# Kernel tuning notes

Measured on AMD Instinct MI355X. Metric: run time of the kernel, lower is better.

## Reference

```python
import jax, jax.numpy as jnp
import numpy as np

WS = 7      # window_size
NH = 8      # num_heads
ND = 5      # n_degree -> Np = 6


def setup_inputs() -> dict:
    key = jax.random.key(0)
    ks = jax.random.split(key, 9)
    B, Q, C, H, W = 2, 100, 256, 64, 64
    Np = ND + 1
    ws2 = WS * WS
    return {
        "x": jax.random.normal(ks[0], (B, C, H, W), dtype=jnp.float32),
        "polys": jax.random.uniform(ks[1], (B, Q, 2, Np), dtype=jnp.float32),
        "w_qkv": jax.random.normal(ks[2], (3 * C, C), dtype=jnp.float32) * 0.02,
        "b_qkv": jnp.zeros((3 * C,), dtype=jnp.float32),
        "w_proj": jax.random.normal(ks[3], (C, C), dtype=jnp.float32) * 0.02,
        "b_proj": jnp.zeros((C,), dtype=jnp.float32),
        "conv_w": jax.random.normal(ks[4], (1, ws2, 1, 1), dtype=jnp.float32) * 0.1,
        "conv_b": jnp.zeros((1,), dtype=jnp.float32),
        "pos_bias": jax.random.normal(ks[5], (ws2, 1), dtype=jnp.float32),
    }


def reference(x, polys, w_qkv, b_qkv, w_proj, b_proj, conv_w, conv_b, pos_bias):
    B, C, H, W = x.shape
    _, Q, _, Np = polys.shape  # polys: [B,Q,2,n_degree+1]
    ws = WS
    ws2 = ws * ws
    nh = NH
    hd = C // nh
    scale = hd ** -0.5

    # --- polynomial -> sample points (get_points) ---
    alpha = jnp.linspace(0.0, 1.0, Np)
    alphas = jnp.stack([alpha ** i for i in range(Np - 1, -1, -1)], axis=1)  # [Np, Np]
    points = jnp.swapaxes(polys @ alphas.T, -1, -2)  # [B,Q,Np,2]
    points = 2.0 * points - 1.0
    points = points[:, :, None, :, :]  # [B,Q,1,Np,2]

    # --- deformable window grid (faithful to torch, incl. -ws//2 floor-div) ---
    lo = (-ws) // 2   # -4 for ws=7
    hi = ws // 2      #  3
    delta_h = 2.0 * jnp.linspace(lo, hi, ws) / H
    delta_w = 2.0 * jnp.linspace(lo, hi, ws) / W
    mesh_x, mesh_y = jnp.meshgrid(delta_w, delta_h, indexing='xy')  # [ws,ws]
    mesh_x = mesh_x.reshape(-1, 1)  # [ws2,1]
    mesh_y = mesh_y.reshape(-1, 1)
    grid_y = points[..., 0] + mesh_y  # [B,Q,ws2,Np]
    grid_x = points[..., 1] + mesh_x
    grid = jnp.stack((grid_y, grid_x), axis=-1)        # [B,Q,ws2,Np,2]
    grid = grid.reshape(B, Q * Np * ws2, 2)            # same flat order as torch .view

    # --- grid_sample: bilinear, zeros padding, align_corners=True ---
    # grid[...,0] -> x coordinate (width), grid[...,1] -> y (height)
    def sample_one(img, g):  # img [C,H,W], g [P,2] -> [C,P]
        fx = (g[:, 0] + 1.0) * 0.5 * (W - 1)
        fy = (g[:, 1] + 1.0) * 0.5 * (H - 1)
        x0 = jnp.floor(fx)
        y0 = jnp.floor(fy)
        wx1 = fx - x0
        wy1 = fy - y0

        def gather(yy, xx):
            valid = (xx >= 0) & (xx <= W - 1) & (yy >= 0) & (yy <= H - 1)
            xi = jnp.clip(xx, 0, W - 1).astype(jnp.int32)
            yi = jnp.clip(yy, 0, H - 1).astype(jnp.int32)
            return img[:, yi, xi] * valid.astype(img.dtype)  # [C,P]

        v00 = gather(y0, x0)
        v01 = gather(y0, x0 + 1)
        v10 = gather(y0 + 1, x0)
        v11 = gather(y0 + 1, x0 + 1)
        return (v00 * (1 - wy1) * (1 - wx1) + v01 * (1 - wy1) * wx1 +
                v10 * wy1 * (1 - wx1) + v11 * wy1 * wx1)

    sampled = jax.vmap(sample_one)(x, grid)            # [B, C, Q*Np*ws2]
    sampled = sampled.reshape(B, C, Q * Np, ws2)
    sampled = jnp.transpose(sampled, (0, 2, 1, 3))     # [B, Q*Np, C, ws2]
    sp = sampled.reshape(B, Q, Np, C, ws2)
    sp = jnp.transpose(sp, (0, 1, 2, 4, 3)).reshape(B, Q * Np, ws2, C)

    # --- windowed multi-head self-attention over each sampled patch ---
    qkv = sp @ w_qkv.T + b_qkv                          # [B,QN,ws2,3C]
    qkv = qkv.reshape(B, Q * Np, ws2, 3, nh, hd)
    qkv = jnp.transpose(qkv, (3, 0, 4, 1, 2, 5))        # [3,B,nh,QN,ws2,hd]
    q, k, v = qkv[0], qkv[1], qkv[2]
    attn = jnp.einsum('bhnpd,bhnqd->bhnpq', q, k) * scale
    attn = attn + pos_bias.reshape(1, 1, 1, ws2, 1)     # bias per query row (as in torch)
    attn = jax.nn.softmax(attn, axis=-1)
    o = jnp.einsum('bhnpq,bhnqd->bhnpd', attn, v)       # [B,nh,QN,ws2,hd]
    o = jnp.swapaxes(o, 2, 3)                           # [B,nh,ws2,QN,hd]
    o = o.reshape(B, Q * Np, ws2, C)                    # faithful torch .reshape
    o = jnp.swapaxes(o, 1, 2)                           # [B,ws2,QN,C]

    # --- conv1x1 over the ws2 channel axis, then output projection ---
    y = jnp.einsum('bwnc,w->bnc', o, conv_w.reshape(ws2)) + conv_b.reshape(1, 1, 1)
    y = y @ w_proj.T + b_proj                           # [B,QN,C]
    return y.reshape(B, Q, Np, C)
```

## Files before the change

kernel.cpp:

```cpp
#include <hip/hip_runtime.h>
#include <hip/hip_bf16.h>

#define B_    2
#define QN    100
#define NP    6
#define WS2   49
#define CC    256
#define NHH   8
#define HDD   32
#define NWIN  600

#define XT_BYTES   (8388608 + 1024)
#define ZABS       2097152
#define WB_BYTES   393216
#define WPT_BYTES  262144

#define SPB_LD 264

#define QK_LD  72
#define VT_LD  72
#define P_LD   72
#define OW_LD  36
#define QK_SHORTS   (WS2 * QK_LD)
#define WREG_SHORTS (QK_SHORTS + 32 * VT_LD)

typedef __attribute__((ext_vector_type(8))) short bf16x8;
typedef __attribute__((ext_vector_type(4))) float f32x4;

__device__ __forceinline__ unsigned short f2bf(float f) {
  return __builtin_bit_cast(unsigned short, __float2bfloat16(f));
}
__device__ __forceinline__ float bf2f(unsigned short u) {
  union { unsigned int i; float f; } v; v.i = ((unsigned int)u) << 16; return v.f;
}

__global__ void k0_prep(const float* __restrict__ x, float* __restrict__ xT,
                        const float* __restrict__ w_qkv, unsigned short* __restrict__ wbp,
                        const float* __restrict__ w_proj, float* __restrict__ wpT) {
  __shared__ float tile[64][65];
  const int gb = blockIdx.x;
  if (gb < 512) {
    int b   = gb >> 8;
    int rem = gb & 255;
    int hw0 = (rem & 63) * 64;
    int c0  = (rem >> 6) * 64;
    int tx = threadIdx.x & 15, ty = threadIdx.x >> 4;
    const float* src = x + (size_t)b * CC * 4096;
    float* dst = xT + (size_t)b * 4096 * CC;
    #pragma unroll
    for (int i = 0; i < 4; i++) {
      int cl = ty + i * 16;
      float4 v = *(const float4*)(src + (size_t)(c0 + cl) * 4096 + hw0 + tx * 4);
      tile[tx * 4 + 0][cl] = v.x;
      tile[tx * 4 + 1][cl] = v.y;
      tile[tx * 4 + 2][cl] = v.z;
      tile[tx * 4 + 3][cl] = v.w;
    }
    __syncthreads();
    #pragma unroll
    for (int i = 0; i < 4; i++) {
      int hl = ty + i * 16;
      float4 v;
      v.x = tile[hl][tx * 4 + 0];
      v.y = tile[hl][tx * 4 + 1];
      v.z = tile[hl][tx * 4 + 2];
      v.w = tile[hl][tx * 4 + 3];
      *(float4*)(dst + (size_t)(hw0 + hl) * 256 + c0 + tx * 4) = v;
    }
  } else if (gb < 608) {
    int g = (gb - 512) * 256 + threadIdx.x;
    int lane = g & 63;
    int ks = (g >> 6) & 7;
    int nt = g >> 9;
    int n  = nt * 16 + (lane & 15);
    int k0 = ks * 32 + (lane >> 4) * 8;
    const float* src = w_qkv + (size_t)n * CC + k0;
    float4 lo = *(const float4*)(src);
    float4 hi = *(const float4*)(src + 4);
    unsigned short o[8] = { f2bf(lo.x), f2bf(lo.y), f2bf(lo.z), f2bf(lo.w),
                            f2bf(hi.x), f2bf(hi.y), f2bf(hi.z), f2bf(hi.w) };
    *(uint4*)(wbp + (size_t)g * 8) = *(uint4*)o;
  } else if (gb == 608) {
    xT[ZABS + threadIdx.x] = 0.0f;
  } else {
    int t = gb - 609;
    int r0 = (t >> 3) * 32;
    int c0 = (t & 7) * 32;
    int tx = threadIdx.x & 31, ty = threadIdx.x >> 5;
    #pragma unroll
    for (int i = ty; i < 32; i += 8)
      tile[i][tx] = w_proj[(size_t)(r0 + i) * CC + c0 + tx];
    __syncthreads();
    #pragma unroll
    for (int i = ty; i < 32; i += 8)
      wpT[(size_t)(c0 + i) * CC + r0 + tx] = tile[tx][i];
  }
}

__device__ __forceinline__ void attn_head(
    const bf16x8 qf[4], const bf16x8 kf[4],
    unsigned short* P, const unsigned short* Vt, float* Ow, unsigned short* ob16,
    int lane, int lm, int lg) {
  const float scale = 0.17677669529663687f;
  f32x4 s[4][4];
  __builtin_amdgcn_s_setprio(1);
  #pragma unroll
  for (int mt = 0; mt < 4; mt++)
    #pragma unroll
    for (int nt = 0; nt < 4; nt++) {
      s[mt][nt] = (f32x4){0.f, 0.f, 0.f, 0.f};
      s[mt][nt] = __builtin_amdgcn_mfma_f32_16x16x32_bf16(qf[mt], kf[nt], s[mt][nt], 0, 0, 0);
    }
  __builtin_amdgcn_s_setprio(0);
  #pragma unroll
  for (int mt = 0; mt < 4; mt++)
    #pragma unroll
    for (int nt = 0; nt < 4; nt++) {
      bool badcol = (nt == 3) && (lm > 0);
      #pragma unroll
      for (int reg = 0; reg < 4; reg++)
        s[mt][nt][reg] = badcol ? -1e30f : s[mt][nt][reg] * scale;
    }
  #pragma unroll
  for (int mt = 0; mt < 4; mt++) {
    #pragma unroll
    for (int reg = 0; reg < 4; reg++) {
      float mx = fmaxf(fmaxf(s[mt][0][reg], s[mt][1][reg]),
                       fmaxf(s[mt][2][reg], s[mt][3][reg]));
      #pragma unroll
      for (int off = 1; off < 16; off <<= 1) mx = fmaxf(mx, __shfl_xor(mx, off));
      float sum = 0.0f;
      #pragma unroll
      for (int nt = 0; nt < 4; nt++) {
        float e = __expf(s[mt][nt][reg] - mx);
        s[mt][nt][reg] = e;
        sum += e;
      }
      #pragma unroll
      for (int off = 1; off < 16; off <<= 1) sum += __shfl_xor(sum, off);
      float inv = 1.0f / sum;
      #pragma unroll
      for (int nt = 0; nt < 4; nt++) s[mt][nt][reg] *= inv;
    }
  }
  #pragma unroll
  for (int mt = 0; mt < 4; mt++)
    #pragma unroll
    for (int nt = 0; nt < 4; nt++)
      #pragma unroll
      for (int reg = 0; reg < 4; reg++) {
        int p = mt * 16 + lg * 4 + reg;
        if (p < WS2) P[p * P_LD + nt * 16 + lm] = f2bf(s[mt][nt][reg]);
      }
  f32x4 o[4][2];
  #pragma unroll
  for (int mt = 0; mt < 4; mt++)
    #pragma unroll
    for (int nt2 = 0; nt2 < 2; nt2++) o[mt][nt2] = (f32x4){0.f, 0.f, 0.f, 0.f};
  #pragma unroll
  for (int ks = 0; ks < 2; ks++) {
    bf16x8 vf[2];
    #pragma unroll
    for (int nt2 = 0; nt2 < 2; nt2++)
      vf[nt2] = *(const bf16x8*)(Vt + (nt2 * 16 + lm) * VT_LD + ks * 32 + lg * 8);
    __builtin_amdgcn_s_setprio(1);
    #pragma unroll
    for (int mt = 0; mt < 4; mt++) {
      bf16x8 af = *(const bf16x8*)(P + (mt * 16 + lm) * P_LD + ks * 32 + lg * 8);
      #pragma unroll
      for (int nt2 = 0; nt2 < 2; nt2++)
        o[mt][nt2] = __builtin_amdgcn_mfma_f32_16x16x32_bf16(af, vf[nt2], o[mt][nt2], 0, 0, 0);
    }
    __builtin_amdgcn_s_setprio(0);
  }
  #pragma unroll
  for (int mt = 0; mt < 4; mt++)
    #pragma unroll
    for (int reg = 0; reg < 4; reg++) {
      int p = mt * 16 + lg * 4 + reg;
      if (p < WS2) {
        #pragma unroll
        for (int nt2 = 0; nt2 < 2; nt2++)
          Ow[p * OW_LD + nt2 * 16 + lm] = o[mt][nt2][reg];
      }
    }
  for (int idx = lane; idx < WS2 * 4; idx += 64) {
    int p = idx >> 2, seg = idx & 3;
    const float* src = Ow + p * OW_LD + seg * 8;
    unsigned short o8[8];
    #pragma unroll
    for (int k = 0; k < 8; k++) o8[k] = f2bf(src[k]);
    *(uint4*)(ob16 + (size_t)idx * 8) = *(uint4*)o8;
  }
}

__launch_bounds__(256, 2)
__global__ void k12_fused(const float* __restrict__ xT,
                          const float* __restrict__ polys,
                          const unsigned short* __restrict__ wbp,
                          const float* __restrict__ b_qkv,
                          unsigned short* __restrict__ o16) {
  __shared__ __align__(16) unsigned short spb[64 * SPB_LD];
  __shared__ __align__(16) unsigned short wreg[4][WREG_SHORTS];
  int*   co_off = (int*)&wreg[0][0];
  float* co_w   = (float*)&wreg[0][0] + 196;
  const int tid = threadIdx.x;
  const int m = (blockIdx.x & 7) * 75 + (blockIdx.x >> 3);
  const int b = blockIdx.y;
  const int lane = tid & 63;
  const int wv = tid >> 6;
  const int lm = lane & 15;
  const int lg = lane >> 4;
  unsigned short* myq = &wreg[wv][0];
  unsigned short* VtW = myq + QK_SHORTS;

  if (tid < WS2) {
    int n = m * WS2 + tid;
    int q = n / (WS2 * NP);
    int p = (n / NP) % WS2;
    int a = n % NP;
    const float* pc = polys + (size_t)(b * QN + q) * 12;
    float al = (float)a * 0.2f;
    float py = pc[0];
    float px = pc[6];
    #pragma unroll
    for (int i = 1; i < 6; i++) { py = py * al + pc[i]; px = px * al + pc[6 + i]; }
    py = 2.0f * py - 1.0f;
    px = 2.0f * px - 1.0f;
    float gy = py + (2.0f * (-4.0f + (float)(p / 7) * (7.0f / 6.0f))) * (1.0f / 64.0f);
    float gx = px + (2.0f * (-4.0f + (float)(p % 7) * (7.0f / 6.0f))) * (1.0f / 64.0f);
    float fx = (gy + 1.0f) * 0.5f * 63.0f;
    float fy = (gx + 1.0f) * 0.5f * 63.0f;
    float x0 = floorf(fx), y0 = floorf(fy);
    float wx = fx - x0, wy = fy - y0;
    float x1 = x0 + 1.0f, y1 = y0 + 1.0f;
    int xi0 = (int)fminf(fmaxf(x0, 0.0f), 63.0f);
    int yi0 = (int)fminf(fmaxf(y0, 0.0f), 63.0f);
    int xi1 = (int)fminf(fmaxf(x1, 0.0f), 63.0f);
    int yi1 = (int)fminf(fmaxf(y1, 0.0f), 63.0f);
    bool vx0 = (x0 >= 0.0f) && (x0 <= 63.0f);
    bool vx1 = (x1 >= 0.0f) && (x1 <= 63.0f);
    bool vy0 = (y0 >= 0.0f) && (y0 <= 63.0f);
    bool vy1 = (y1 >= 0.0f) && (y1 <= 63.0f);
    const int bb = b * 4096;
    co_off[tid * 4 + 0] = (vx0 && vy0) ? (bb + yi0 * 64 + xi0) * CC : ZABS;
    co_off[tid * 4 + 1] = (vx1 && vy0) ? (bb + yi0 * 64 + xi1) * CC : ZABS;
    co_off[tid * 4 + 2] = (vx0 && vy1) ? (bb + yi1 * 64 + xi0) * CC : ZABS;
    co_off[tid * 4 + 3] = (vx1 && vy1) ? (bb + yi1 * 64 + xi1) * CC : ZABS;
    co_w[tid * 4 + 0] = (1.0f - wy) * (1.0f - wx);
    co_w[tid * 4 + 1] = (1.0f - wy) * wx;
    co_w[tid * 4 + 2] = wy * (1.0f - wx);
    co_w[tid * 4 + 3] = wy * wx;
  }
  {
    unsigned int* z = (unsigned int*)(spb + WS2 * SPB_LD);
    for (int i = tid; i < 15 * SPB_LD / 2; i += 256) z[i] = 0u;
  }
  {
    unsigned int* vz = (unsigned int*)VtW;
    #pragma unroll
    for (int i = 0; i < 18; i++) vz[i * 64 + lane] = 0u;
  }
  __syncthreads();

  for (int bi = 0; bi < 6; bi++) {
    const int rbase = bi * 8;
    float vv[8][4];
    #pragma unroll
    for (int k = 0; k < 8; k++) {
      int r = rbase + k;
      int4 off = *(const int4*)&co_off[r * 4];
      vv[k][0] = xT[off.x + tid];
      vv[k][1] = xT[off.y + tid];
      vv[k][2] = xT[off.z + tid];
      vv[k][3] = xT[off.w + tid];
    }
    #pragma unroll
    for (int k = 0; k < 8; k++) {
      int r = rbase + k;
      float4 w = *(const float4*)&co_w[r * 4];
      float s = vv[k][0] * w.x + vv[k][1] * w.y + vv[k][2] * w.z + vv[k][3] * w.w;
      spb[r * SPB_LD + tid] = f2bf(s);
    }
  }
  {
    int4 off = *(const int4*)&co_off[48 * 4];
    float4 w = *(const float4*)&co_w[48 * 4];
    float s = xT[off.x + tid] * w.x + xT[off.y + tid] * w.y
            + xT[off.z + tid] * w.z + xT[off.w + tid] * w.w;
    spb[48 * SPB_LD + tid] = f2bf(s);
  }
  __syncthreads();

  unsigned short* obase = o16 + (size_t)(b * NWIN + m) * 392 * 32;

  for (int hp = 0; hp < 2; hp++) {
    const int h = 2 * wv + hp;
    for (int jc = 0; jc < 3; jc++) {
      const int nt0 = jc * 16 + 2 * h;
      f32x4 acc[4][2];
      #pragma unroll
      for (int j4 = 0; j4 < 2; j4++) {
        float bias = b_qkv[(nt0 + j4) * 16 + lm];
        #pragma unroll
        for (int mt = 0; mt < 4; mt++) acc[mt][j4] = (f32x4){bias, bias, bias, bias};
      }
      bf16x8 bnx[2][2];
      #pragma unroll
      for (int j4 = 0; j4 < 2; j4++) {
        bnx[0][j4] = *(const bf16x8*)(wbp + (size_t)(((nt0 + j4) * 8 + 0) * 64 + lane) * 8);
        bnx[1][j4] = *(const bf16x8*)(wbp + (size_t)(((nt0 + j4) * 8 + 1) * 64 + lane) * 8);
      }
      #pragma unroll
      for (int ks = 0; ks < 8; ks++) {
        bf16x8 bc[2];
        #pragma unroll
        for (int j4 = 0; j4 < 2; j4++) bc[j4] = bnx[ks & 1][j4];
        if (ks < 6) {
          #pragma unroll
          for (int j4 = 0; j4 < 2; j4++)
            bnx[ks & 1][j4] = *(const bf16x8*)(wbp + (size_t)(((nt0 + j4) * 8 + ks + 2) * 64 + lane) * 8);
        }
        bf16x8 af[4];
        #pragma unroll
        for (int mt = 0; mt < 4; mt++)
          af[mt] = *(const bf16x8*)(spb + (mt * 16 + lm) * SPB_LD + ks * 32 + lg * 8);
        __builtin_amdgcn_s_setprio(1);
        #pragma unroll
        for (int j4 = 0; j4 < 2; j4++)
          #pragma unroll
          for (int mt = 0; mt < 4; mt++)
            acc[mt][j4] = __builtin_amdgcn_mfma_f32_16x16x32_bf16(af[mt], bc[j4], acc[mt][j4], 0, 0, 0);
        __builtin_amdgcn_s_setprio(0);
      }
      if (jc < 2) {
        const int cb = jc * 32;
        #pragma unroll
        for (int mt = 0; mt < 4; mt++)
          #pragma unroll
          for (int reg = 0; reg < 4; reg++) {
            int rr = mt * 16 + lg * 4 + reg;
            if (rr < WS2) {
              #pragma unroll
              for (int j4 = 0; j4 < 2; j4++)
                myq[rr * QK_LD + cb + j4 * 16 + lm] = f2bf(acc[mt][j4][reg]);
            }
          }
      } else {
        #pragma unroll
        for (int mt = 0; mt < 4; mt++)
          #pragma unroll
          for (int reg = 0; reg < 4; reg++) {
            int rr = mt * 16 + lg * 4 + reg;
            if (rr < WS2) {
              #pragma unroll
              for (int j4 = 0; j4 < 2; j4++)
                VtW[(j4 * 16 + lm) * VT_LD + rr] = f2bf(acc[mt][j4][reg]);
            }
          }
      }
    }

    bf16x8 qf[4], kf[4];
    #pragma unroll
    for (int t = 0; t < 4; t++) {
      int r = t * 16 + lm; if (r > 48) r = 48;
      const unsigned short* row = myq + r * QK_LD;
      qf[t] = *(const bf16x8*)(row + lg * 8);
      kf[t] = *(const bf16x8*)(row + 32 + lg * 8);
    }
    unsigned short* P = myq;
    float* Ow = (float*)myq;
    attn_head(qf, kf, P, VtW, Ow,
              obase + (size_t)h * WS2 * HDD, lane, lm, lg);
  }
}

__global__ void k3_conv_proj(const unsigned short* __restrict__ o16,
                             const float* __restrict__ conv_w,
                             const float* __restrict__ conv_b,
                             const float* __restrict__ wpT,
                             const float* __restrict__ b_proj,
                             float* __restrict__ out) {
  __shared__ float yv[2][CC];
  __shared__ float cw[WS2];
  __shared__ int atab[2][392];
  const int tid = threadIdx.x;
  const int orig = blockIdx.x;
  const int xcd = orig & 7;
  const int sub = orig >> 3;
  const int wg = (xcd < 4 ? xcd * 38 : 152 + (xcd - 4) * 37) + sub;
  const int np0 = wg * 2;
  const int b = blockIdx.y;
  if (tid < WS2) cw[tid] = conv_w[tid];
  for (int i = tid; i < 784; i += 256) {
    int which = (i >= 392) ? 1 : 0;
    int ii = i - which * 392;
    int Q = (np0 + which) * 392 + ii;
    int mq = Q % 600;
    int hp = Q / 600;
    atab[which][ii] = ((b * NWIN + mq) * 392 + hp) * 32;
  }
  __syncthreads();
  const int cg = tid >> 5, dd = tid & 31;
  float acc0 = conv_b[0], acc1 = conv_b[0];
  #pragma unroll 1
  for (int pb = 0; pb < 48; pb += 8) {
    float v0[8], v1[8];
    #pragma unroll
    for (int k = 0; k < 8; k++) {
      v0[k] = bf2f(o16[(size_t)atab[0][(pb + k) * 8 + cg] + dd]);
      v1[k] = bf2f(o16[(size_t)atab[1][(pb + k) * 8 + cg] + dd]);
    }
    #pragma unroll
    for (int k = 0; k < 8; k++) {
      acc0 += cw[pb + k] * v0[k];
      acc1 += cw[pb + k] * v1[k];
    }
  }
  acc0 += cw[48] * bf2f(o16[(size_t)atab[0][48 * 8 + cg] + dd]);
  acc1 += cw[48] * bf2f(o16[(size_t)atab[1][48 * 8 + cg] + dd]);
  yv[0][tid] = acc0;
  yv[1][tid] = acc1;
  __syncthreads();
  const float* wp = wpT + tid;
  float a0 = 0.0f, a1 = 0.0f, c0 = 0.0f, c1 = 0.0f;
  #pragma unroll 8
  for (int c = 0; c < CC; c += 2) {
    float w0 = wp[(c + 0) * CC];
    float w1 = wp[(c + 1) * CC];
    a0 += yv[0][c] * w0;  a1 += yv[0][c + 1] * w1;
    c0 += yv[1][c] * w0;  c1 += yv[1][c + 1] * w1;
  }
  float bp = b_proj[tid];
  out[((size_t)(b * NWIN + np0)) * CC + tid]     = bp + (a0 + a1);
  out[((size_t)(b * NWIN + np0 + 1)) * CC + tid] = bp + (c0 + c1);
}

extern "C" void kernel_launch(void* const* d_in, const int* in_sizes, int n_in,
                              void* d_out, int out_size, void* d_ws, size_t ws_size,
                              hipStream_t stream) {
  const float* x        = (const float*)d_in[0];
  const float* polys    = (const float*)d_in[1];
  const float* w_qkv    = (const float*)d_in[2];
  const float* b_qkv    = (const float*)d_in[3];
  const float* w_proj   = (const float*)d_in[4];
  const float* b_proj   = (const float*)d_in[5];
  const float* conv_w   = (const float*)d_in[6];
  const float* conv_b   = (const float*)d_in[7];
  float* out = (float*)d_out;

  char* ws = (char*)d_ws;
  float* xT = (float*)ws;
  unsigned short* wbp = (unsigned short*)(ws + XT_BYTES);
  float* wpT = (float*)(ws + XT_BYTES + WB_BYTES);
  unsigned short* o16 = (unsigned short*)(ws + XT_BYTES + WB_BYTES + WPT_BYTES);

  hipLaunchKernelGGL(k0_prep, dim3(673), dim3(256), 0, stream, x, xT, w_qkv, wbp, w_proj, wpT);
  hipLaunchKernelGGL(k12_fused, dim3(NWIN, B_), dim3(256), 0, stream,
                     xT, polys, wbp, b_qkv, o16);
  hipLaunchKernelGGL(k3_conv_proj, dim3(300, B_), dim3(256), 0, stream,
                     o16, conv_w, conv_b, wpT, b_proj, out);
}
```

Measured before the change: 158.6 us.

## Keep V in registers via shuffles and XOR-swizzle per-wave LDS to shrink footprint

Result: slower. 162.4 us (+2.4%).

```diff
diff --git a/kernel.cpp b/kernel.cpp
--- a/kernel.cpp
+++ b/kernel.cpp
@@ -17,21 +17,20 @@
 
 #define SPB_LD 264
 
-#define QK_LD  72
-#define VT_LD  72
-#define P_LD   72
-#define OW_LD  36
-#define QK_SHORTS   (WS2 * QK_LD)
-#define WREG_SHORTS (QK_SHORTS + 32 * VT_LD)
+#define RG_SHORTS (WS2 * 64)
 
 typedef __attribute__((ext_vector_type(8))) short bf16x8;
 typedef __attribute__((ext_vector_type(4))) float f32x4;
+typedef __attribute__((ext_vector_type(4))) unsigned int u32x4;
 
 __device__ __forceinline__ unsigned short f2bf(float f) {
   return __builtin_bit_cast(unsigned short, __float2bfloat16(f));
 }
 __device__ __forceinline__ float bf2f(unsigned short u) {
   union { unsigned int i; float f; } v; v.i = ((unsigned int)u) << 16; return v.f;
+}
+__device__ __forceinline__ unsigned int pk2(float a, float b) {
+  return (unsigned int)f2bf(a) | ((unsigned int)f2bf(b) << 16);
 }
 
 __global__ void k0_prep(const float* __restrict__ x, float* __restrict__ xT,
@@ -97,113 +96,16 @@
   }
 }
 
-__device__ __forceinline__ void attn_head(
-    const bf16x8 qf[4], const bf16x8 kf[4],
-    unsigned short* P, const unsigned short* Vt, float* Ow, unsigned short* ob16,
-    int lane, int lm, int lg) {
-  const float scale = 0.17677669529663687f;
-  f32x4 s[4][4];
-  __builtin_amdgcn_s_setprio(1);
-  #pragma unroll
-  for (int mt = 0; mt < 4; mt++)
-    #pragma unroll
-    for (int nt = 0; nt < 4; nt++) {
-      s[mt][nt] = (f32x4){0.f, 0.f, 0.f, 0.f};
-      s[mt][nt] = __builtin_amdgcn_mfma_f32_16x16x32_bf16(qf[mt], kf[nt], s[mt][nt], 0, 0, 0);
-    }
-  __builtin_amdgcn_s_setprio(0);
-  #pragma unroll
-  for (int mt = 0; mt < 4; mt++)
-    #pragma unroll
-    for (int nt = 0; nt < 4; nt++) {
-      bool badcol = (nt == 3) && (lm > 0);
-      #pragma unroll
-      for (int reg = 0; reg < 4; reg++)
-        s[mt][nt][reg] = badcol ? -1e30f : s[mt][nt][reg] * scale;
-    }
-  #pragma unroll
-  for (int mt = 0; mt < 4; mt++) {
-    #pragma unroll
-    for (int reg = 0; reg < 4; reg++) {
-      float mx = fmaxf(fmaxf(s[mt][0][reg], s[mt][1][reg]),
-                       fmaxf(s[mt][2][reg], s[mt][3][reg]));
-      #pragma unroll
-      for (int off = 1; off < 16; off <<= 1) mx = fmaxf(mx, __shfl_xor(mx, off));
-      float sum = 0.0f;
-      #pragma unroll
-      for (int nt = 0; nt < 4; nt++) {
-        float e = __expf(s[mt][nt][reg] - mx);
-        s[mt][nt][reg] = e;
-        sum += e;
-      }
-      #pragma unroll
-      for (int off = 1; off < 16; off <<= 1) sum += __shfl_xor(sum, off);
-      float inv = 1.0f / sum;
-      #pragma unroll
-      for (int nt = 0; nt < 4; nt++) s[mt][nt][reg] *= inv;
-    }
-  }
-  #pragma unroll
-  for (int mt = 0; mt < 4; mt++)
-    #pragma unroll
-    for (int nt = 0; nt < 4; nt++)
-      #pragma unroll
-      for (int reg = 0; reg < 4; reg++) {
-        int p = mt * 16 + lg * 4 + reg;
-        if (p < WS2) P[p * P_LD + nt * 16 + lm] = f2bf(s[mt][nt][reg]);
-      }
-  f32x4 o[4][2];
-  #pragma unroll
-  for (int mt = 0; mt < 4; mt++)
-    #pragma unroll
-    for (int nt2 = 0; nt2 < 2; nt2++) o[mt][nt2] = (f32x4){0.f, 0.f, 0.f, 0.f};
-  #pragma unroll
-  for (int ks = 0; ks < 2; ks++) {
-    bf16x8 vf[2];
-    #pragma unroll
-    for (int nt2 = 0; nt2 < 2; nt2++)
-      vf[nt2] = *(const bf16x8*)(Vt + (nt2 * 16 + lm) * VT_LD + ks * 32 + lg * 8);
-    __builtin_amdgcn_s_setprio(1);
-    #pragma unroll
-    for (int mt = 0; mt < 4; mt++) {
-      bf16x8 af = *(const bf16x8*)(P + (mt * 16 + lm) * P_LD + ks * 32 + lg * 8);
-      #pragma unroll
-      for (int nt2 = 0; nt2 < 2; nt2++)
-        o[mt][nt2] = __builtin_amdgcn_mfma_f32_16x16x32_bf16(af, vf[nt2], o[mt][nt2], 0, 0, 0);
-    }
-    __builtin_amdgcn_s_setprio(0);
-  }
-  #pragma unroll
-  for (int mt = 0; mt < 4; mt++)
-    #pragma unroll
-    for (int reg = 0; reg < 4; reg++) {
-      int p = mt * 16 + lg * 4 + reg;
-      if (p < WS2) {
-        #pragma unroll
-        for (int nt2 = 0; nt2 < 2; nt2++)
-          Ow[p * OW_LD + nt2 * 16 + lm] = o[mt][nt2][reg];
-      }
-    }
-  for (int idx = lane; idx < WS2 * 4; idx += 64) {
-    int p = idx >> 2, seg = idx & 3;
-    const float* src = Ow + p * OW_LD + seg * 8;
-    unsigned short o8[8];
-    #pragma unroll
-    for (int k = 0; k < 8; k++) o8[k] = f2bf(src[k]);
-    *(uint4*)(ob16 + (size_t)idx * 8) = *(uint4*)o8;
-  }
-}
-
 __launch_bounds__(256, 2)
 __global__ void k12_fused(const float* __restrict__ xT,
                           const float* __restrict__ polys,
                           const unsigned short* __restrict__ wbp,
                           const float* __restrict__ b_qkv,
                           unsigned short* __restrict__ o16) {
-  __shared__ __align__(16) unsigned short spb[64 * SPB_LD];
-  __shared__ __align__(16) unsigned short wreg[4][WREG_SHORTS];
-  int*   co_off = (int*)&wreg[0][0];
-  float* co_w   = (float*)&wreg[0][0] + 196;
+  __shared__ __align__(16) unsigned short spb[WS2 * SPB_LD];
+  __shared__ __align__(16) unsigned short wreg[4 * RG_SHORTS];
+  int*   co_off = (int*)wreg;
+  float* co_w   = (float*)wreg + 196;
   const int tid = threadIdx.x;
   const int m = (blockIdx.x & 7) * 75 + (blockIdx.x >> 3);
   const int b = blockIdx.y;
@@ -211,8 +113,7 @@
   const int wv = tid >> 6;
   const int lm = lane & 15;
   const int lg = lane >> 4;
-  unsigned short* myq = &wreg[wv][0];
-  unsigned short* VtW = myq + QK_SHORTS;
+  unsigned short* myreg = wreg + wv * RG_SHORTS;
 
   if (tid < WS2) {
     int n = m * WS2 + tid;
@@ -252,15 +153,6 @@
     co_w[tid * 4 + 2] = wy * (1.0f - wx);
     co_w[tid * 4 + 3] = wy * wx;
   }
-  {
-    unsigned int* z = (unsigned int*)(spb + WS2 * SPB_LD);
-    for (int i = tid; i < 15 * SPB_LD / 2; i += 256) z[i] = 0u;
-  }
-  {
-    unsigned int* vz = (unsigned int*)VtW;
-    #pragma unroll
-    for (int i = 0; i < 18; i++) vz[i * 64 + lane] = 0u;
-  }
   __syncthreads();
 
   for (int bi = 0; bi < 6; bi++) {
@@ -292,10 +184,20 @@
   }
   __syncthreads();
 
+  int rowb[4];
+  #pragma unroll
+  for (int mt = 0; mt < 4; mt++) {
+    int r = mt * 16 + lm; if (r > 48) r = 48;
+    rowb[mt] = r * SPB_LD;
+  }
+
   unsigned short* obase = o16 + (size_t)(b * NWIN + m) * 392 * 32;
+  const float scale = 0.17677669529663687f;
 
   for (int hp = 0; hp < 2; hp++) {
     const int h = 2 * wv + hp;
+    unsigned int vpk[4][2][2];
+
     for (int jc = 0; jc < 3; jc++) {
       const int nt0 = jc * 16 + 2 * h;
       f32x4 acc[4][2];
@@ -324,7 +226,7 @@
         bf16x8 af[4];
         #pragma unroll
         for (int mt = 0; mt < 4; mt++)
-          af[mt] = *(const bf16x8*)(spb + (mt * 16 + lm) * SPB_LD + ks * 32 + lg * 8);
+          af[mt] = *(const bf16x8*)(spb + rowb[mt] + ks * 32 + lg * 8);
         __builtin_amdgcn_s_setprio(1);
         #pragma unroll
         for (int j4 = 0; j4 < 2; j4++)
@@ -342,21 +244,19 @@
             int rr = mt * 16 + lg * 4 + reg;
             if (rr < WS2) {
               #pragma unroll
-              for (int j4 = 0; j4 < 2; j4++)
-                myq[rr * QK_LD + cb + j4 * 16 + lm] = f2bf(acc[mt][j4][reg]);
+              for (int j4 = 0; j4 < 2; j4++) {
+                int c = cb + j4 * 16 + lm;
+                myreg[rr * 64 + ((((c >> 3) ^ (rr & 7)) << 3) | (c & 7))] = f2bf(acc[mt][j4][reg]);
+              }
             }
           }
       } else {
         #pragma unroll
         for (int mt = 0; mt < 4; mt++)
           #pragma unroll
-          for (int reg = 0; reg < 4; reg++) {
-            int rr = mt * 16 + lg * 4 + reg;
-            if (rr < WS2) {
-              #pragma unroll
-              for (int j4 = 0; j4 < 2; j4++)
-                VtW[(j4 * 16 + lm) * VT_LD + rr] = f2bf(acc[mt][j4][reg]);
-            }
+          for (int j4 = 0; j4 < 2; j4++) {
+            vpk[mt][j4][0] = pk2(acc[mt][j4][0], acc[mt][j4][1]);
+            vpk[mt][j4][1] = pk2(acc[mt][j4][2], acc[mt][j4][3]);
           }
       }
     }
@@ -365,14 +265,124 @@
     #pragma unroll
     for (int t = 0; t < 4; t++) {
       int r = t * 16 + lm; if (r > 48) r = 48;
-      const unsigned short* row = myq + r * QK_LD;
-      qf[t] = *(const bf16x8*)(row + lg * 8);
-      kf[t] = *(const bf16x8*)(row + 32 + lg * 8);
-    }
-    unsigned short* P = myq;
-    float* Ow = (float*)myq;
-    attn_head(qf, kf, P, VtW, Ow,
-              obase + (size_t)h * WS2 * HDD, lane, lm, lg);
+      const unsigned short* row = myreg + r * 64;
+      qf[t] = *(const bf16x8*)(row + ((lg ^ (r & 7)) << 3));
+      kf[t] = *(const bf16x8*)(row + (((4 + lg) ^ (r & 7)) << 3));
+    }
+
+    f32x4 s[4][4];
+    __builtin_amdgcn_s_setprio(1);
+    #pragma unroll
+    for (int mt = 0; mt < 4; mt++)
+      #pragma unroll
+      for (int nt = 0; nt < 4; nt++) {
+        s[mt][nt] = (f32x4){0.f, 0.f, 0.f, 0.f};
+        s[mt][nt] = __builtin_amdgcn_mfma_f32_16x16x32_bf16(qf[mt], kf[nt], s[mt][nt], 0, 0, 0);
+      }
+    __builtin_amdgcn_s_setprio(0);
+    #pragma unroll
+    for (int mt = 0; mt < 4; mt++)
+      #pragma unroll
+      for (int nt = 0; nt < 4; nt++) {
+        bool badcol = (nt == 3) && (lm > 0);
+        #pragma unroll
+        for (int reg = 0; reg < 4; reg++)
+          s[mt][nt][reg] = badcol ? -1e30f : s[mt][nt][reg] * scale;
+      }
+    #pragma unroll
+    for (int mt = 0; mt < 4; mt++) {
+      #pragma unroll
+      for (int reg = 0; reg < 4; reg++) {
+        float mx = fmaxf(fmaxf(s[mt][0][reg], s[mt][1][reg]),
+                         fmaxf(s[mt][2][reg], s[mt][3][reg]));
+        #pragma unroll
+        for (int off = 1; off < 16; off <<= 1) mx = fmaxf(mx, __shfl_xor(mx, off));
+        float sum = 0.0f;
+        #pragma unroll
+        for (int nt = 0; nt < 4; nt++) {
+          float e = __expf(s[mt][nt][reg] - mx);
+          s[mt][nt][reg] = e;
+          sum += e;
+        }
+        #pragma unroll
+        for (int off = 1; off < 16; off <<= 1) sum += __shfl_xor(sum, off);
+        float inv = 1.0f / sum;
+        #pragma unroll
+        for (int nt = 0; nt < 4; nt++) s[mt][nt][reg] *= inv;
+      }
+    }
+    #pragma unroll
+    for (int mt = 0; mt < 4; mt++)
+      #pragma unroll
+      for (int nt = 0; nt < 4; nt++)
+        #pragma unroll
+        for (int reg = 0; reg < 4; reg++) {
+          int p = mt * 16 + lg * 4 + reg;
+          if (p < WS2) {
+            int c = nt * 16 + lm;
+            myreg[p * 64 + ((((c >> 3) ^ (p & 7)) << 3) | (c & 7))] = f2bf(s[mt][nt][reg]);
+          }
+        }
+    f32x4 o[4][2];
+    #pragma unroll
+    for (int mt = 0; mt < 4; mt++)
+      #pragma unroll
+      for (int nt2 = 0; nt2 < 2; nt2++) o[mt][nt2] = (f32x4){0.f, 0.f, 0.f, 0.f};
+    const int sA = (lane & 15) + ((lane >> 4) & 1) * 32;
+    const int sB = sA + 16;
+    const int hi = (lane >> 5) & 1;
+    #pragma unroll
+    for (int ks = 0; ks < 2; ks++) {
+      bf16x8 vf[2];
+      #pragma unroll
+      for (int nt2 = 0; nt2 < 2; nt2++) {
+        unsigned w0a = __shfl(vpk[2 * ks + 0][nt2][0], sA);
+        unsigned w0b = __shfl(vpk[2 * ks + 1][nt2][0], sA);
+        unsigned w1a = __shfl(vpk[2 * ks + 0][nt2][1], sA);
+        unsigned w1b = __shfl(vpk[2 * ks + 1][nt2][1], sA);
+        unsigned w2a = __shfl(vpk[2 * ks + 0][nt2][0], sB);
+        unsigned w2b = __shfl(vpk[2 * ks + 1][nt2][0], sB);
+        unsigned w3a = __shfl(vpk[2 * ks + 0][nt2][1], sB);
+        unsigned w3b = __shfl(vpk[2 * ks + 1][nt2][1], sB);
+        u32x4 uv;
+        uv.x = hi ? w0b : w0a;
+        uv.y = hi ? w1b : w1a;
+        uv.z = hi ? w2b : w2a;
+        uv.w = hi ? w3b : w3a;
+        vf[nt2] = __builtin_bit_cast(bf16x8, uv);
+      }
+      __builtin_amdgcn_s_setprio(1);
+      #pragma unroll
+      for (int mt = 0; mt < 4; mt++) {
+        int r = mt * 16 + lm; if (r > 48) r = 48;
+        bf16x8 af = *(const bf16x8*)(myreg + r * 64 + (((ks * 4 + lg) ^ (r & 7)) << 3));
+        #pragma unroll
+        for (int nt2 = 0; nt2 < 2; nt2++)
+          o[mt][nt2] = __builtin_amdgcn_mfma_f32_16x16x32_bf16(af, vf[nt2], o[mt][nt2], 0, 0, 0);
+      }
+      __builtin_amdgcn_s_setprio(0);
+    }
+    float* Ow = (float*)myreg;
+    #pragma unroll
+    for (int mt = 0; mt < 4; mt++)
+      #pragma unroll
+      for (int reg = 0; reg < 4; reg++) {
+        int p = mt * 16 + lg * 4 + reg;
+        if (p < WS2) {
+          #pragma unroll
+          for (int nt2 = 0; nt2 < 2; nt2++)
+            Ow[p * 32 + nt2 * 16 + lm] = o[mt][nt2][reg];
+        }
+      }
+    unsigned short* ob16 = obase + (size_t)h * WS2 * HDD;
+    for (int idx = lane; idx < WS2 * 4; idx += 64) {
+      int p = idx >> 2, seg = idx & 3;
+      const float* src = Ow + p * 32 + seg * 8;
+      unsigned short o8[8];
+      #pragma unroll
+      for (int k = 0; k < 8; k++) o8[k] = f2bf(src[k]);
+      *(uint4*)(ob16 + (size_t)idx * 8) = *(uint4*)o8;
+    }
   }
 }
 
```
